# Performance work log

Hardware: AMD Instinct MI355X
Metric: run time of the kernel (lower is better)

## Reference

```python
import jax, jax.numpy as jnp
import numpy as np

_DN = ('NCHW', 'OIHW', 'NCHW')


def _gaussian_kernel1d(ksize, sigma):
    x = np.arange(ksize, dtype=np.float32) - ksize // 2
    g = np.exp(-x ** 2 / (2.0 * sigma ** 2))
    return (g / g.sum()).astype(np.float32)


def _nms_kernels():
    # kornia get_canny_nms_kernel: kernel k = center - neighbor at angle k*45deg (0deg = +x/right)
    k = np.zeros((8, 1, 3, 3), dtype=np.float32)
    offs = [(0, 1), (-1, 1), (-1, 0), (-1, -1), (0, -1), (1, -1), (1, 0), (1, 1)]
    for i, (dy, dx) in enumerate(offs):
        k[i, 0, 1, 1] = 1.0
        k[i, 0, 1 + dy, 1 + dx] = -1.0
    return k


def _conv(x, w, padding):
    return jax.lax.conv_general_dilated(x, w, (1, 1), padding, dimension_numbers=_DN)


def _canny_magnitude(data):
    eps = 1e-6
    x = (data + 1.0) / 2.0
    # rgb -> grayscale (kornia weights)
    rgb_w = jnp.array([0.299, 0.587, 0.114], dtype=x.dtype)
    gray = jnp.einsum('bchw,c->bhw', x, rgb_w)[:, None]  # [B,1,H,W]
    # gaussian blur 5x5, sigma=1, reflect border (kornia default), separable
    g1d = jnp.asarray(_gaussian_kernel1d(5, 1.0), dtype=x.dtype)
    p = jnp.pad(gray, ((0, 0), (0, 0), (2, 2), (2, 2)), mode='reflect')
    blurred = _conv(_conv(p, g1d.reshape(1, 1, 1, 5), 'VALID'), g1d.reshape(1, 1, 5, 1), 'VALID')
    # sobel spatial gradient (normalized=False), replicate padding
    sob_x = jnp.array([[-1., 0., 1.], [-2., 0., 2.], [-1., 0., 1.]], dtype=x.dtype)
    sob = jnp.stack([sob_x, sob_x.T])[:, None]  # [2,1,3,3]
    bp = jnp.pad(blurred, ((0, 0), (0, 0), (1, 1), (1, 1)), mode='edge')
    grads = _conv(bp, sob, 'VALID')  # [B,2,H,W]
    gx, gy = grads[:, 0:1], grads[:, 1:2]
    magnitude = jnp.sqrt(gx * gx + gy * gy + eps)  # [B,1,H,W]
    # angle rounded to nearest 45 degrees
    ang45 = jnp.round(jnp.rad2deg(jnp.arctan2(gy, gx)) / 45.0)
    # non-maximum suppression: center-minus-neighbor along 8 directions (zero pad)
    nms_k = jnp.asarray(_nms_kernels(), dtype=x.dtype)
    nms_mag = _conv(magnitude, nms_k, ((1, 1), (1, 1)))  # [B,8,H,W]
    idx_pos = ang45.astype(jnp.int32) % 8
    idx_neg = (idx_pos + 4) % 8
    sel_pos = jnp.take_along_axis(nms_mag, idx_pos, axis=1)
    sel_neg = jnp.take_along_axis(nms_mag, idx_neg, axis=1)
    is_max = jnp.minimum(sel_pos, sel_neg) > 0.0
    return magnitude * is_max


def setup_inputs() -> dict:
    key = jax.random.key(0)
    data = jax.random.normal(key, (16, 3, 512, 512), dtype=jnp.float32)
    return {'data': data}


def reference(data):
    # EdgeOperator.forward: canny((data+1)/2)[0] -> NMS'd gradient magnitude [B,1,H,W]
    return _canny_magnitude(data)
```

## Files before the change

kernel.cpp:

```cpp
#include <hip/hip_runtime.h>
#include <math.h>

#define IMH 512
#define IMW 512
#define T   32
#define GS  40
#define BS  36
#define MS  34

#define LG  44
#define OG  0
#define LH  37
#define OH  1760
#define LB  37
#define OB  3240
#define LM  35
#define OM  4572
#define LX  33
#define OGX 0
#define OGY 1056
#define NPOOL 5762

__device__ __forceinline__ int reflect_i(int v, int n) {
    if (v < 0) v = -v;
    if (v >= n) v = 2 * n - 2 - v;
    return v;
}
__device__ __forceinline__ int clamp_i(int v, int n) {
    return v < 0 ? 0 : (v >= n ? n - 1 : v);
}

__global__ __launch_bounds__(256)
void canny_mag_kernel(const float* __restrict__ data, float* __restrict__ out) {
    __shared__ float sP[NPOOL];
    const int bx0 = blockIdx.x * T;
    const int by0 = blockIdx.y * T;
    const int b   = blockIdx.z;
    const int tid = threadIdx.x;
    const bool xin = (bx0 >= 4) && (bx0 + T + 4 <= IMW);
    const bool bin = (bx0 >= 1) && (bx0 + T + 1 <= IMW) &&
                     (by0 >= 1) && (by0 + T + 1 <= IMH);

    const float w0 = 0.05448868f, w1 = 0.24420134f, w2 = 0.40261995f;
    const size_t plane = (size_t)IMH * IMW;
    const float* p0 = data + (size_t)b * 3 * plane;
    const float* p1 = p0 + plane;
    const float* p2 = p1 + plane;

    if (xin) {
        for (int idx = tid; idx < GS * 10; idx += 256) {
            int r = idx / 10, c4 = idx - r * 10;
            int ry = reflect_i(by0 - 4 + r, IMH);
            int off = ry * IMW + (bx0 - 4) + c4 * 4;
            const float4 a = *(const float4*)(p0 + off);
            const float4 g = *(const float4*)(p1 + off);
            const float4 c = *(const float4*)(p2 + off);
            float4 o;
            o.x = 0.1495f * a.x + 0.2935f * g.x + 0.057f * c.x + 0.5f;
            o.y = 0.1495f * a.y + 0.2935f * g.y + 0.057f * c.y + 0.5f;
            o.z = 0.1495f * a.z + 0.2935f * g.z + 0.057f * c.z + 0.5f;
            o.w = 0.1495f * a.w + 0.2935f * g.w + 0.057f * c.w + 0.5f;
            *(float4*)&sP[OG + r * LG + c4 * 4] = o;
        }
    } else {
        for (int idx = tid; idx < GS * GS; idx += 256) {
            int i = idx / GS, j = idx - i * GS;
            int ry = reflect_i(by0 - 4 + i, IMH);
            int rx = reflect_i(bx0 - 4 + j, IMW);
            int off = ry * IMW + rx;
            sP[OG + i * LG + j] = 0.1495f * p0[off] + 0.2935f * p1[off] + 0.057f * p2[off] + 0.5f;
        }
    }
    __syncthreads();

    for (int idx = tid; idx < GS * BS; idx += 256) {
        int i = idx / BS, j = idx - i * BS;
        int cj = xin ? (j + 2) : (clamp_i(bx0 - 2 + j, IMW) - bx0 + 4);
        const float* g = &sP[OG + i * LG + cj];
        sP[OH + i * LH + j] = w0 * (g[-2] + g[2]) + w1 * (g[-1] + g[1]) + w2 * g[0];
    }
    __syncthreads();

    for (int idx = tid; idx < BS * BS; idx += 256) {
        int jy = idx / BS, jx = idx - jy * BS;
        int ci = clamp_i(by0 - 2 + jy, IMH) - by0 + 4;
        const float* h = &sP[OH + ci * LH + jx];
        sP[OB + jy * LB + jx] = w0 * (h[-2 * LH] + h[2 * LH]) + w1 * (h[-LH] + h[LH]) + w2 * h[0];
    }
    __syncthreads();

    for (int idx = tid; idx < MS * MS; idx += 256) {
        int iy = idx / MS, ix = idx - iy * MS;
        const float* bb = &sP[OB + (iy + 1) * LB + (ix + 1)];
        float a00 = bb[-LB - 1], a01 = bb[-LB], a02 = bb[-LB + 1];
        float a10 = bb[-1],                      a12 = bb[1];
        float a20 = bb[LB - 1],  a21 = bb[LB],  a22 = bb[LB + 1];
        float gx = (a02 - a00) + 2.0f * (a12 - a10) + (a22 - a20);
        float gy = (a20 - a00) + 2.0f * (a21 - a01) + (a22 - a02);
        float m = sqrtf(gx * gx + gy * gy + 1e-6f);
        if (!bin) {
            int my = by0 - 1 + iy, mx = bx0 - 1 + ix;
            if (my < 0 || my >= IMH || mx < 0 || mx >= IMW) m = 0.0f;
        }
        sP[OM + iy * LM + ix] = m;
        int iyy = iy - 1, ixx = ix - 1;
        if ((unsigned)iyy < 32u && (unsigned)ixx < 32u) {
            sP[OGX + iyy * LX + ixx] = gx;
            sP[OGY + iyy * LX + ixx] = gy;
        }
    }
    __syncthreads();

    const int lx  = tid & 31;
    const int lyb = tid >> 5;
    size_t obase = (size_t)b * plane + (size_t)(by0 + lyb) * IMW + (bx0 + lx);
    for (int r = 0; r < 4; ++r) {
        int ly = lyb + 8 * r;
        float mag = sP[OM + (ly + 1) * LM + (lx + 1)];
        float gx = sP[OGX + ly * LX + lx];
        float gy = sP[OGY + ly * LX + lx];
        float ax = fabsf(gx), ay = fabsf(gy);
        int dy, dx;
        if (ay <= 0.41421356237f * ax)      { dy = 0; dx = 1; }
        else if (ay >= 2.41421356237f * ax) { dy = 1; dx = 0; }
        else                                { dx = 1; dy = (gx * gy > 0.0f) ? -1 : 1; }
        float n1 = sP[OM + (ly + 1 + dy) * LM + (lx + 1 + dx)];
        float n2 = sP[OM + (ly + 1 - dy) * LM + (lx + 1 - dx)];
        float o = (mag > n1 && mag > n2) ? mag : 0.0f;
        out[obase + (size_t)(8 * r) * IMW] = o;
    }
}

extern "C" void kernel_launch(void* const* d_in, const int* in_sizes, int n_in,
                              void* d_out, int out_size, void* d_ws, size_t ws_size,
                              hipStream_t stream) {
    const float* data = (const float*)d_in[0];
    float* out = (float*)d_out;
    int B = in_sizes[0] / (3 * IMH * IMW);
    dim3 grid(IMW / T, IMH / T, B);
    canny_mag_kernel<<<grid, dim3(256, 1, 1), 0, stream>>>(data, out);
}
```

Baseline: 104.2 us.

## Vectorize blur, Sobel, and NMS stages with float4 LDS accesses

Re-pads the shared-memory intermediate buffers to 16-byte-aligned strides so that each stage (horizontal blur, vertical blur, Sobel/magnitude, NMS) processes four adjacent pixels per thread using float4 LDS loads and stores. The final output is written as a single float4 per thread instead of four strided scalar stores. The aim is to cut LDS instruction count and integer index math. In exchange, shared memory use grows, the intermediate arrays take a shifted column layout, and aligned strides may add bank conflicts.

Result: no change. 104.5 us (+0.3%).

```diff
diff --git a/kernel.cpp b/kernel.cpp
--- a/kernel.cpp
+++ b/kernel.cpp
@@ -5,21 +5,19 @@
 #define IMW 512
 #define T   32
 #define GS  40
-#define BS  36
-#define MS  34
 
 #define LG  44
 #define OG  0
-#define LH  37
+#define LH  40
 #define OH  1760
-#define LB  37
-#define OB  3240
-#define LM  35
-#define OM  4572
-#define LX  33
+#define LB  40
+#define OB  3360
+#define LM  40
+#define OM  4800
+#define LX  32
 #define OGX 0
-#define OGY 1056
-#define NPOOL 5762
+#define OGY 1024
+#define NPOOL 6160
 
 __device__ __forceinline__ int reflect_i(int v, int n) {
     if (v < 0) v = -v;
@@ -32,7 +30,7 @@
 
 __global__ __launch_bounds__(256)
 void canny_mag_kernel(const float* __restrict__ data, float* __restrict__ out) {
-    __shared__ float sP[NPOOL];
+    __shared__ __align__(16) float sP[NPOOL];
     const int bx0 = blockIdx.x * T;
     const int by0 = blockIdx.y * T;
     const int b   = blockIdx.z;
@@ -73,61 +71,109 @@
     }
     __syncthreads();
 
-    for (int idx = tid; idx < GS * BS; idx += 256) {
-        int i = idx / BS, j = idx - i * BS;
-        int cj = xin ? (j + 2) : (clamp_i(bx0 - 2 + j, IMW) - bx0 + 4);
-        const float* g = &sP[OG + i * LG + cj];
-        sP[OH + i * LH + j] = w0 * (g[-2] + g[2]) + w1 * (g[-1] + g[1]) + w2 * g[0];
-    }
-    __syncthreads();
-
-    for (int idx = tid; idx < BS * BS; idx += 256) {
-        int jy = idx / BS, jx = idx - jy * BS;
-        int ci = clamp_i(by0 - 2 + jy, IMH) - by0 + 4;
-        const float* h = &sP[OH + ci * LH + jx];
-        sP[OB + jy * LB + jx] = w0 * (h[-2 * LH] + h[2 * LH]) + w1 * (h[-LH] + h[LH]) + w2 * h[0];
-    }
-    __syncthreads();
-
-    for (int idx = tid; idx < MS * MS; idx += 256) {
-        int iy = idx / MS, ix = idx - iy * MS;
-        const float* bb = &sP[OB + (iy + 1) * LB + (ix + 1)];
-        float a00 = bb[-LB - 1], a01 = bb[-LB], a02 = bb[-LB + 1];
-        float a10 = bb[-1],                      a12 = bb[1];
-        float a20 = bb[LB - 1],  a21 = bb[LB],  a22 = bb[LB + 1];
-        float gx = (a02 - a00) + 2.0f * (a12 - a10) + (a22 - a20);
-        float gy = (a20 - a00) + 2.0f * (a21 - a01) + (a22 - a02);
-        float m = sqrtf(gx * gx + gy * gy + 1e-6f);
-        if (!bin) {
-            int my = by0 - 1 + iy, mx = bx0 - 1 + ix;
-            if (my < 0 || my >= IMH || mx < 0 || mx >= IMW) m = 0.0f;
+    if (xin) {
+        for (int idx = tid; idx < GS * 9; idx += 256) {
+            int i = idx / 9, gq = idx - i * 9;
+            const float4 A = *(const float4*)&sP[OG + i * LG + 4 * gq];
+            const float4 Bv = *(const float4*)&sP[OG + i * LG + 4 * gq + 4];
+            float W0 = A.x, W1 = A.y, W2 = A.z, W3 = A.w;
+            float W4 = Bv.x, W5 = Bv.y, W6 = Bv.z, W7 = Bv.w;
+            float4 o;
+            o.x = w0 * (W0 + W4) + w1 * (W1 + W3) + w2 * W2;
+            o.y = w0 * (W1 + W5) + w1 * (W2 + W4) + w2 * W3;
+            o.z = w0 * (W2 + W6) + w1 * (W3 + W5) + w2 * W4;
+            o.w = w0 * (W3 + W7) + w1 * (W4 + W6) + w2 * W5;
+            *(float4*)&sP[OH + i * LH + 4 * gq] = o;
         }
-        sP[OM + iy * LM + ix] = m;
-        int iyy = iy - 1, ixx = ix - 1;
-        if ((unsigned)iyy < 32u && (unsigned)ixx < 32u) {
-            sP[OGX + iyy * LX + ixx] = gx;
-            sP[OGY + iyy * LX + ixx] = gy;
+    } else {
+        for (int idx = tid; idx < GS * 36; idx += 256) {
+            int i = idx / 36, j = idx - i * 36;
+            int cj = clamp_i(bx0 - 2 + j, IMW) - bx0 + 4;
+            const float* gp = &sP[OG + i * LG + cj];
+            sP[OH + i * LH + j] = w0 * (gp[-2] + gp[2]) + w1 * (gp[-1] + gp[1]) + w2 * gp[0];
         }
     }
     __syncthreads();
 
-    const int lx  = tid & 31;
-    const int lyb = tid >> 5;
-    size_t obase = (size_t)b * plane + (size_t)(by0 + lyb) * IMW + (bx0 + lx);
-    for (int r = 0; r < 4; ++r) {
-        int ly = lyb + 8 * r;
-        float mag = sP[OM + (ly + 1) * LM + (lx + 1)];
-        float gx = sP[OGX + ly * LX + lx];
-        float gy = sP[OGY + ly * LX + lx];
-        float ax = fabsf(gx), ay = fabsf(gy);
-        int dy, dx;
-        if (ay <= 0.41421356237f * ax)      { dy = 0; dx = 1; }
-        else if (ay >= 2.41421356237f * ax) { dy = 1; dx = 0; }
-        else                                { dx = 1; dy = (gx * gy > 0.0f) ? -1 : 1; }
-        float n1 = sP[OM + (ly + 1 + dy) * LM + (lx + 1 + dx)];
-        float n2 = sP[OM + (ly + 1 - dy) * LM + (lx + 1 - dx)];
-        float o = (mag > n1 && mag > n2) ? mag : 0.0f;
-        out[obase + (size_t)(8 * r) * IMW] = o;
+    for (int idx = tid; idx < 36 * 9; idx += 256) {
+        int jy = idx / 9, gq = idx - jy * 9;
+        int ci = clamp_i(by0 - 2 + jy, IMH) - by0 + 4;
+        int base = OH + ci * LH + 4 * gq;
+        const float4 r0 = *(const float4*)&sP[base - 2 * LH];
+        const float4 r1 = *(const float4*)&sP[base - LH];
+        const float4 r2 = *(const float4*)&sP[base];
+        const float4 r3 = *(const float4*)&sP[base + LH];
+        const float4 r4 = *(const float4*)&sP[base + 2 * LH];
+        float4 o;
+        o.x = w0 * (r0.x + r4.x) + w1 * (r1.x + r3.x) + w2 * r2.x;
+        o.y = w0 * (r0.y + r4.y) + w1 * (r1.y + r3.y) + w2 * r2.y;
+        o.z = w0 * (r0.z + r4.z) + w1 * (r1.z + r3.z) + w2 * r2.z;
+        o.w = w0 * (r0.w + r4.w) + w1 * (r1.w + r3.w) + w2 * r2.w;
+        *(float4*)&sP[OB + jy * LB + 4 * gq + 4] = o;
+    }
+    __syncthreads();
+
+    for (int idx = tid; idx < 34 * 10; idx += 256) {
+        int iy = idx / 10, gq = idx - iy * 10;
+        int baseB = OB + iy * LB + 4 * gq;
+        const float4 t0a = *(const float4*)&sP[baseB];
+        const float4 t0b = *(const float4*)&sP[baseB + 4];
+        const float4 t1a = *(const float4*)&sP[baseB + LB];
+        const float4 t1b = *(const float4*)&sP[baseB + LB + 4];
+        const float4 t2a = *(const float4*)&sP[baseB + 2 * LB];
+        const float4 t2b = *(const float4*)&sP[baseB + 2 * LB + 4];
+        float W0[8] = {t0a.x, t0a.y, t0a.z, t0a.w, t0b.x, t0b.y, t0b.z, t0b.w};
+        float W1[8] = {t1a.x, t1a.y, t1a.z, t1a.w, t1b.x, t1b.y, t1b.z, t1b.w};
+        float W2[8] = {t2a.x, t2a.y, t2a.z, t2a.w, t2b.x, t2b.y, t2b.z, t2b.w};
+        float mg[4], gxv[4], gyv[4];
+        #pragma unroll
+        for (int k = 0; k < 4; ++k) {
+            float a00 = W0[k + 1], a01 = W0[k + 2], a02 = W0[k + 3];
+            float a10 = W1[k + 1],                  a12 = W1[k + 3];
+            float a20 = W2[k + 1], a21 = W2[k + 2], a22 = W2[k + 3];
+            float gx = (a02 - a00) + 2.0f * (a12 - a10) + (a22 - a20);
+            float gy = (a20 - a00) + 2.0f * (a21 - a01) + (a22 - a02);
+            float m = sqrtf(gx * gx + gy * gy + 1e-6f);
+            if (!bin) {
+                int my = by0 - 1 + iy;
+                int cx = bx0 - 4 + 4 * gq + k;
+                if (my < 0 || my >= IMH || cx < 0 || cx >= IMW) m = 0.0f;
+            }
+            mg[k] = m; gxv[k] = gx; gyv[k] = gy;
+        }
+        *(float4*)&sP[OM + iy * LM + 4 * gq] = make_float4(mg[0], mg[1], mg[2], mg[3]);
+        if (gq >= 1 && gq <= 8 && iy >= 1 && iy <= 32) {
+            int st = (iy - 1) * LX + 4 * gq - 4;
+            *(float4*)&sP[OGX + st] = make_float4(gxv[0], gxv[1], gxv[2], gxv[3]);
+            *(float4*)&sP[OGY + st] = make_float4(gyv[0], gyv[1], gyv[2], gyv[3]);
+        }
+    }
+    __syncthreads();
+
+    {
+        const int ly  = tid >> 3;
+        const int lx0 = (tid & 7) * 4;
+        const float4 mag4 = *(const float4*)&sP[OM + (ly + 1) * LM + lx0 + 4];
+        const float4 gx4  = *(const float4*)&sP[OGX + ly * LX + lx0];
+        const float4 gy4  = *(const float4*)&sP[OGY + ly * LX + lx0];
+        const float magv[4] = {mag4.x, mag4.y, mag4.z, mag4.w};
+        const float gxv2[4] = {gx4.x, gx4.y, gx4.z, gx4.w};
+        const float gyv2[4] = {gy4.x, gy4.y, gy4.z, gy4.w};
+        float ov[4];
+        #pragma unroll
+        for (int k = 0; k < 4; ++k) {
+            float gx = gxv2[k], gy = gyv2[k], mag = magv[k];
+            float ax = fabsf(gx), ay = fabsf(gy);
+            int dy, dx;
+            if (ay <= 0.41421356237f * ax)      { dy = 0; dx = 1; }
+            else if (ay >= 2.41421356237f * ax) { dy = 1; dx = 0; }
+            else                                { dx = 1; dy = (gx * gy > 0.0f) ? -1 : 1; }
+            float n1 = sP[OM + (ly + 1 + dy) * LM + (lx0 + k + 4 + dx)];
+            float n2 = sP[OM + (ly + 1 - dy) * LM + (lx0 + k + 4 - dx)];
+            ov[k] = (mag > n1 && mag > n2) ? mag : 0.0f;
+        }
+        float4 o4 = make_float4(ov[0], ov[1], ov[2], ov[3]);
+        *(float4*)&out[(size_t)b * plane + (size_t)(by0 + ly) * IMW + (bx0 + lx0)] = o4;
     }
 }
 
```
